# Performance work log

Hardware: AMD Instinct MI355X
Metric: run time of the kernel (lower is better)

The kernel has to match this reference:

```python
import jax, jax.numpy as jnp
import numpy as np

N_QUBITS = 4


def _apply_rx(state, theta, wire):
    # state: [B, 2,2,2,2] complex64, theta: [B] real angles; RX on `wire`.
    st = jnp.moveaxis(state, wire + 1, -1)
    bshape = (theta.shape[0],) + (1,) * (st.ndim - 2)
    c = jnp.cos(theta * 0.5).reshape(bshape).astype(jnp.complex64)
    s = (-1j) * jnp.sin(theta * 0.5).reshape(bshape).astype(jnp.complex64)
    new = jnp.stack([c * st[..., 0] + s * st[..., 1],
                     s * st[..., 0] + c * st[..., 1]], axis=-1)
    return jnp.moveaxis(new, -1, wire + 1)


def _apply_cnot(state, control, target):
    st = jnp.moveaxis(state, (control + 1, target + 1), (-2, -1))
    new = jnp.stack([st[..., 0, :], st[..., 1, ::-1]], axis=-2)
    return jnp.moveaxis(new, (-2, -1), (control + 1, target + 1))


def _quantum_gate(angles, thetas):
    # angles: [B, n] data-encoding RX angles; thetas: [n] trainable RX angles.
    B, n = angles.shape
    state = jnp.zeros((B,) + (2,) * n, jnp.complex64)
    state = state.at[(slice(None),) + (0,) * n].set(1.0)  # |0...0>
    for w in range(n):
        state = _apply_rx(state, angles[:, w], w)
    for w in range(n):
        state = _apply_rx(state, jnp.broadcast_to(thetas[w], (B,)), w)
    for w in range(n):
        state = _apply_cnot(state, w, (w + 1) % n)
    probs = jnp.abs(state.reshape(B, 2 ** n)) ** 2  # [B, 16]
    bits = (np.arange(2 ** n)[:, None] >> np.arange(n - 1, -1, -1)[None, :]) & 1
    signs = jnp.asarray(1.0 - 2.0 * bits, jnp.float32)  # [16, n] PauliZ eigvals
    return probs @ signs  # [B, n] <Z_w> expectations


def setup_inputs() -> dict:
    key = jax.random.key(0)
    ks = jax.random.split(key, 12)
    B, D, H, n = 131072, 256, 4, N_QUBITS
    fan_in = D + H
    sc = 1.0 / np.sqrt(fan_in)
    inp = {
        'x': jax.random.normal(ks[0], (B, D), jnp.float32),
        'hx': jax.random.normal(ks[1], (B, H), jnp.float32),
        'cx': jax.random.normal(ks[2], (B, H), jnp.float32),
        'W_f': jax.random.normal(ks[3], (n, fan_in), jnp.float32) * sc,
        'b_f': jnp.zeros((n,), jnp.float32),
        'W_i': jax.random.normal(ks[4], (n, fan_in), jnp.float32) * sc,
        'b_i': jnp.zeros((n,), jnp.float32),
        'W_u': jax.random.normal(ks[5], (n, fan_in), jnp.float32) * sc,
        'b_u': jnp.zeros((n,), jnp.float32),
        'W_o': jax.random.normal(ks[6], (n, fan_in), jnp.float32) * sc,
        'b_o': jnp.zeros((n,), jnp.float32),
        'th_f': jax.random.normal(ks[7], (n,), jnp.float32),
        'th_i': jax.random.normal(ks[8], (n,), jnp.float32),
        'th_u': jax.random.normal(ks[9], (n,), jnp.float32),
        'th_o': jax.random.normal(ks[10], (n,), jnp.float32),
    }
    return inp


def reference(x, hx, cx, W_f, b_f, W_i, b_i, W_u, b_u, W_o, b_o,
              th_f, th_i, th_u, th_o):
    comb = jnp.concatenate([x, hx], axis=1)  # [B, D+H]
    f = jax.nn.sigmoid(_quantum_gate(comb @ W_f.T + b_f, th_f))
    i = jax.nn.sigmoid(_quantum_gate(comb @ W_i.T + b_i, th_i))
    g = jnp.tanh(_quantum_gate(comb @ W_u.T + b_u, th_u))
    o = jax.nn.sigmoid(_quantum_gate(comb @ W_o.T + b_o, th_o))
    c_new = f * cx + i * g
    h_new = o * jnp.tanh(c_new)
    return (h_new, c_new)
```

## Files before the change

### kernel.cpp

```cpp
#include <hip/hip_runtime.h>

#define NB    131072
#define TPB   256
#define FANIN 260

__device__ __forceinline__ float sigm_(float x) { return 1.0f / (1.0f + __expf(-x)); }
__device__ __forceinline__ float tanh_(float x) { return 1.0f - 2.0f / (__expf(2.0f * x) + 1.0f); }

__global__ void qlstm_prep(const float* __restrict__ Wf, const float* __restrict__ bf,
                           const float* __restrict__ Wi, const float* __restrict__ bi,
                           const float* __restrict__ Wu, const float* __restrict__ bu,
                           const float* __restrict__ Wo, const float* __restrict__ bo,
                           const float* __restrict__ thf, const float* __restrict__ thi,
                           const float* __restrict__ thu, const float* __restrict__ tho,
                           float* __restrict__ Wp, float* __restrict__ bth) {
    int t = blockIdx.x * blockDim.x + threadIdx.x;
    if (t < FANIN * 16) {
        int k = t >> 4, gw = t & 15, g = gw >> 2, w = gw & 3;
        const float* Wg = (g == 0) ? Wf : (g == 1) ? Wi : (g == 2) ? Wu : Wo;
        Wp[t] = Wg[w * FANIN + k];
    }
    if (t < 16) {
        int g = t >> 2, w = t & 3;
        const float* bg = (g == 0) ? bf  : (g == 1) ? bi  : (g == 2) ? bu  : bo;
        const float* tg = (g == 0) ? thf : (g == 1) ? thi : (g == 2) ? thu : tho;
        bth[t] = bg[w] + tg[w];
    }
}

__global__ __launch_bounds__(TPB, 4) void qlstm_main(
        const float* __restrict__ x, const float* __restrict__ hx,
        const float* __restrict__ cx, const float* __restrict__ Wp,
        const float* __restrict__ bth, float* __restrict__ out) {
    __shared__ float accx[16 * 3 * 64];

    const int tid  = threadIdx.x;
    const int lane = tid & 63;
    const int wv   = tid >> 6;
    const int wvu  = __builtin_amdgcn_readfirstlane(wv);
    const int row0 = blockIdx.x * 64;
    const int row  = row0 + lane;

    const float4* xr = (const float4*)x + (size_t)row * 64 + wvu * 16;

    float4 xb[16];
#pragma unroll
    for (int u = 0; u < 16; ++u) xb[u] = xr[u];

    float4 hv  = make_float4(0.f, 0.f, 0.f, 0.f);
    float4 cxv = make_float4(0.f, 0.f, 0.f, 0.f);
    if (wvu == 3) hv  = ((const float4*)hx)[row];
    if (wvu == 0) cxv = ((const float4*)cx)[row];

    float acc[16];
#pragma unroll
    for (int j = 0; j < 16; ++j) acc[j] = 0.0f;

    const float* wbase = Wp + wvu * 64 * 16;
#pragma unroll
    for (int c4 = 0; c4 < 16; ++c4) {
#pragma unroll
        for (int m = 0; m < 4; ++m) {
            float xe = (m == 0) ? xb[c4].x : (m == 1) ? xb[c4].y
                     : (m == 2) ? xb[c4].z : xb[c4].w;
            const float* wp = wbase + (c4 * 4 + m) * 16;
#pragma unroll
            for (int j = 0; j < 16; ++j) acc[j] = fmaf(xe, wp[j], acc[j]);
        }
    }

    if (wvu == 3) {
        const float* wp = Wp + 256 * 16;
#pragma unroll
        for (int j = 0; j < 16; ++j) acc[j] = fmaf(hv.x, wp[j],      acc[j]);
#pragma unroll
        for (int j = 0; j < 16; ++j) acc[j] = fmaf(hv.y, wp[16 + j], acc[j]);
#pragma unroll
        for (int j = 0; j < 16; ++j) acc[j] = fmaf(hv.z, wp[32 + j], acc[j]);
#pragma unroll
        for (int j = 0; j < 16; ++j) acc[j] = fmaf(hv.w, wp[48 + j], acc[j]);
    }

    if (wvu != 0) {
#pragma unroll
        for (int j = 0; j < 16; ++j)
            accx[(j * 3 + (wvu - 1)) * 64 + lane] = acc[j];
    }
    __syncthreads();

    if (wvu == 0) {
#pragma unroll
        for (int j = 0; j < 16; ++j)
            acc[j] += accx[(j * 3 + 0) * 64 + lane]
                    + accx[(j * 3 + 1) * 64 + lane]
                    + accx[(j * 3 + 2) * 64 + lane];

        float co[16];
#pragma unroll
        for (int j = 0; j < 16; ++j) co[j] = __cosf(acc[j] + bth[j]);

        float G[16];
#pragma unroll
        for (int g = 0; g < 4; ++g) {
            float c0 = co[g * 4 + 0], c1 = co[g * 4 + 1];
            float c2 = co[g * 4 + 2], c3 = co[g * 4 + 3];
            float e1 = c0 * c1;
            float e2 = e1 * c2;
            float e3 = e2 * c3;
            float e0 = c1 * c2 * c3;
            G[g * 4 + 0] = e0; G[g * 4 + 1] = e1; G[g * 4 + 2] = e2; G[g * 4 + 3] = e3;
        }

        float cxa[4] = {cxv.x, cxv.y, cxv.z, cxv.w};
        float hn[4], cn[4];
#pragma unroll
        for (int w = 0; w < 4; ++w) {
            float fg = sigm_(G[0 * 4 + w]);
            float ig = sigm_(G[1 * 4 + w]);
            float ug = tanh_(G[2 * 4 + w]);
            float og = sigm_(G[3 * 4 + w]);
            float c_ = fg * cxa[w] + ig * ug;
            cn[w] = c_;
            hn[w] = og * tanh_(c_);
        }

        ((float4*)out)[row]      = make_float4(hn[0], hn[1], hn[2], hn[3]);
        ((float4*)out)[NB + row] = make_float4(cn[0], cn[1], cn[2], cn[3]);
    }
}

extern "C" void kernel_launch(void* const* d_in, const int* in_sizes, int n_in,
                              void* d_out, int out_size, void* d_ws, size_t ws_size,
                              hipStream_t stream) {
    const float* x   = (const float*)d_in[0];
    const float* hx  = (const float*)d_in[1];
    const float* cx  = (const float*)d_in[2];
    const float* Wf  = (const float*)d_in[3];
    const float* bf  = (const float*)d_in[4];
    const float* Wi  = (const float*)d_in[5];
    const float* bi  = (const float*)d_in[6];
    const float* Wu  = (const float*)d_in[7];
    const float* bu  = (const float*)d_in[8];
    const float* Wo  = (const float*)d_in[9];
    const float* bo  = (const float*)d_in[10];
    const float* thf = (const float*)d_in[11];
    const float* thi = (const float*)d_in[12];
    const float* thu = (const float*)d_in[13];
    const float* tho = (const float*)d_in[14];

    float* Wp  = (float*)d_ws;
    float* bth = Wp + FANIN * 16;

    qlstm_prep<<<(FANIN * 16 + 255) / 256, 256, 0, stream>>>(
        Wf, bf, Wi, bi, Wu, bu, Wo, bo, thf, thi, thu, tho, Wp, bth);

    qlstm_main<<<NB / 64, TPB, 0, stream>>>(
        x, hx, cx, Wp, bth, (float*)d_out);
}
```

Measured before the change: 223.5 us.

## Stage x tile through LDS with direct global-to-LDS loads and 8 waves

Replaces per-lane strided float4 loads of x (each lane reading its own row) with global_load_lds so that each wave loads whole rows coalesced into a 64 KB XOR-swizzled LDS tile. Lanes then read their row back from LDS with the swizzle to avoid bank conflicts. Block size doubles to 512 threads, so the reduction dimension is split across 8 waves and the cross-wave LDS reduction grows to 7 partials. The goal is better global coalescing, at the cost of heavy LDS use per block, which limits occupancy, plus extra barriers.

```diff
diff --git a/kernel.cpp b/kernel.cpp
--- a/kernel.cpp
+++ b/kernel.cpp
@@ -1,11 +1,17 @@
 #include <hip/hip_runtime.h>
 
 #define NB    131072
-#define TPB   256
+#define TPB   512
 #define FANIN 260
 
 __device__ __forceinline__ float sigm_(float x) { return 1.0f / (1.0f + __expf(-x)); }
 __device__ __forceinline__ float tanh_(float x) { return 1.0f - 2.0f / (__expf(2.0f * x) + 1.0f); }
+
+__device__ __forceinline__ void gld_lds16(const float4* gsrc, float4* ldst) {
+    __builtin_amdgcn_global_load_lds(
+        (const __attribute__((address_space(1))) void*)gsrc,
+        (__attribute__((address_space(3))) void*)ldst, 16, 0, 0);
+}
 
 __global__ void qlstm_prep(const float* __restrict__ Wf, const float* __restrict__ bf,
                            const float* __restrict__ Wi, const float* __restrict__ bi,
@@ -32,7 +38,7 @@
         const float* __restrict__ x, const float* __restrict__ hx,
         const float* __restrict__ cx, const float* __restrict__ Wp,
         const float* __restrict__ bth, float* __restrict__ out) {
-    __shared__ float accx[16 * 3 * 64];
+    __shared__ float4 xt[64 * 64];
 
     const int tid  = threadIdx.x;
     const int lane = tid & 63;
@@ -41,35 +47,39 @@
     const int row0 = blockIdx.x * 64;
     const int row  = row0 + lane;
 
-    const float4* xr = (const float4*)x + (size_t)row * 64 + wvu * 16;
-
-    float4 xb[16];
-#pragma unroll
-    for (int u = 0; u < 16; ++u) xb[u] = xr[u];
+    const float4* x4 = (const float4*)x + (size_t)row0 * 64;
 
     float4 hv  = make_float4(0.f, 0.f, 0.f, 0.f);
     float4 cxv = make_float4(0.f, 0.f, 0.f, 0.f);
-    if (wvu == 3) hv  = ((const float4*)hx)[row];
+    if (wvu == 7) hv  = ((const float4*)hx)[row];
     if (wvu == 0) cxv = ((const float4*)cx)[row];
+
+#pragma unroll
+    for (int i = 0; i < 8; ++i) {
+        const int r = wvu * 8 + i;
+        gld_lds16(x4 + (size_t)r * 64 + (lane ^ (r & 7)), &xt[r * 64]);
+    }
+    asm volatile("s_waitcnt vmcnt(0)" ::: "memory");
+    __syncthreads();
 
     float acc[16];
 #pragma unroll
     for (int j = 0; j < 16; ++j) acc[j] = 0.0f;
 
-    const float* wbase = Wp + wvu * 64 * 16;
+    const float* wbase = Wp + wvu * 32 * 16;
 #pragma unroll
-    for (int c4 = 0; c4 < 16; ++c4) {
+    for (int j = 0; j < 8; ++j) {
+        float4 xv = xt[lane * 64 + ((wvu * 8 + j) ^ (lane & 7))];
 #pragma unroll
         for (int m = 0; m < 4; ++m) {
-            float xe = (m == 0) ? xb[c4].x : (m == 1) ? xb[c4].y
-                     : (m == 2) ? xb[c4].z : xb[c4].w;
-            const float* wp = wbase + (c4 * 4 + m) * 16;
+            float xe = (m == 0) ? xv.x : (m == 1) ? xv.y : (m == 2) ? xv.z : xv.w;
+            const float* wp = wbase + (j * 4 + m) * 16;
 #pragma unroll
-            for (int j = 0; j < 16; ++j) acc[j] = fmaf(xe, wp[j], acc[j]);
+            for (int jj = 0; jj < 16; ++jj) acc[jj] = fmaf(xe, wp[jj], acc[jj]);
         }
     }
 
-    if (wvu == 3) {
+    if (wvu == 7) {
         const float* wp = Wp + 256 * 16;
 #pragma unroll
         for (int j = 0; j < 16; ++j) acc[j] = fmaf(hv.x, wp[j],      acc[j]);
@@ -81,19 +91,23 @@
         for (int j = 0; j < 16; ++j) acc[j] = fmaf(hv.w, wp[48 + j], acc[j]);
     }
 
+    __syncthreads();
+    float* accx = (float*)xt;
     if (wvu != 0) {
 #pragma unroll
         for (int j = 0; j < 16; ++j)
-            accx[(j * 3 + (wvu - 1)) * 64 + lane] = acc[j];
+            accx[(j * 7 + (wvu - 1)) * 64 + lane] = acc[j];
     }
     __syncthreads();
 
     if (wvu == 0) {
 #pragma unroll
-        for (int j = 0; j < 16; ++j)
-            acc[j] += accx[(j * 3 + 0) * 64 + lane]
-                    + accx[(j * 3 + 1) * 64 + lane]
-                    + accx[(j * 3 + 2) * 64 + lane];
+        for (int j = 0; j < 16; ++j) {
+            float s = acc[j];
+#pragma unroll
+            for (int p = 0; p < 7; ++p) s += accx[(j * 7 + p) * 64 + lane];
+            acc[j] = s;
+        }
 
         float co[16];
 #pragma unroll
```

New measurement: 225.8 us. About the same (+1.0%).
